# Optimization experiments

Hardware: AMD Instinct MI355X
Metric: run time of the kernel (lower is better)

Reference implementation:

```python
import jax, jax.numpy as jnp
import numpy as np

# Channel layout assumed by the model's CH dict
CH_ELEV, CH_WS, CH_WD, CH_HUM, CH_NDVI, CH_FIRE = 0, 1, 2, 3, 4, 5
P_BURN, W_WIND, W_SLOPE = 0.58, 0.045, 0.078
OFFSETS = [(-1, 0), (-1, 1), (0, 1), (1, 1), (1, 0), (1, -1), (0, -1), (-1, -1)]
DIR_ANGLES = [90.0, 45.0, 0.0, 315.0, 270.0, 225.0, 180.0, 135.0]
SOBEL_X = np.array([[-1, 0, 1], [-2, 0, 2], [-1, 0, 1]], np.float32) / 8.0
SOBEL_Y = np.array([[-1, -2, -1], [0, 0, 0], [1, 2, 1]], np.float32) / 8.0


def setup_inputs() -> dict:
    key = jax.random.key(0)
    x = jax.random.uniform(key, (16, 6, 1024, 1024), dtype=jnp.float32)
    return {"x": x}


def _conv2d_same(img, k):
    # img: (B,1,H,W), k: (3,3)
    kern = jnp.asarray(k).reshape(1, 1, 3, 3)
    return jax.lax.conv_general_dilated(img, kern, (1, 1), ((1, 1), (1, 1)))


def _shift(mask, dr, dc):
    # mask: (B,H,W) float; zero-padded shift matching torch slicing
    B, H, W = mask.shape
    p = jnp.pad(mask, ((0, 0), (1, 1), (1, 1)))
    return p[:, 1 + dr:1 + dr + H, 1 + dc:1 + dc + W]


def reference(x):
    B, C, H, W = x.shape
    elev = x[:, CH_ELEV:CH_ELEV + 1]          # (B,1,H,W)
    ws = x[:, CH_WS]                           # (B,H,W)
    wd = x[:, CH_WD]
    hum = x[:, CH_HUM]
    ndvi = x[:, CH_NDVI]
    fs = x[:, CH_FIRE]

    dx = _conv2d_same(elev, SOBEL_X)
    dy = _conv2d_same(elev, SOBEL_Y)
    grad_mag = jnp.sqrt(dx * dx + dy * dy + 1e-8)
    slope = (jnp.arctan(grad_mag) * (180.0 / np.pi))[:, 0]  # (B,H,W) degrees

    burning = (fs > 0.5).astype(x.dtype)
    wind_math = jnp.mod(270.0 - wd, 360.0)
    slope_effect = 1.0 + W_SLOPE * jnp.tan(slope * (np.pi / 180.0))
    moisture_damp = jnp.clip(1.0 - 2.0 * hum * 200.0, 0.3, 1.0)
    veg_factor = 0.5 + 0.5 * jnp.clip(ndvi, 0.0, 1.0)
    base = P_BURN * slope_effect * moisture_damp * veg_factor  # wind-independent part

    prob = jnp.zeros((B, H, W), dtype=x.dtype)
    for (dr, dc), d_angle in zip(OFFSETS, DIR_ANGLES):
        shifted = _shift(burning, dr, dc)
        angle_diff = (d_angle - wind_math) * (np.pi / 180.0)
        wind_factor = 1.0 + W_WIND * jnp.cos(angle_diff) * ws
        p_spread = jnp.clip(base * wind_factor, 0.0, 1.0)
        prob = jnp.maximum(prob, shifted * p_spread)

    unburned = (fs < 0.5).astype(x.dtype)
    out = jnp.maximum(fs, prob * unburned)
    return out[:, None]  # (B,1,H,W)
```

## Files before the change

### kernel.cpp

```cpp
#include <hip/hip_runtime.h>

namespace {
constexpr int CH = 6;
constexpr int H  = 1024;
constexpr int W  = 1024;
constexpr float P_BURN  = 0.58f;
constexpr float W_WIND  = 0.045f;
constexpr float W_SLOPE = 0.078f;
constexpr float C45     = 0.70710678118654752f;
constexpr float DEG2RAD = 0.017453292519943295f;

__device__ __forceinline__ void load6(const float* __restrict__ plane, int row,
                                      int j0, float v[6]) {
    if ((unsigned)row >= (unsigned)H) {
        v[0] = v[1] = v[2] = v[3] = v[4] = v[5] = 0.f;
        return;
    }
    const float* r = plane + (size_t)row * W;
    const float4 m = *reinterpret_cast<const float4*>(r + j0);
    v[0] = (j0 > 0)     ? r[j0 - 1] : 0.f;
    v[1] = m.x; v[2] = m.y; v[3] = m.z; v[4] = m.w;
    v[5] = (j0 + 4 < W) ? r[j0 + 4] : 0.f;
}
}

__global__ __launch_bounds__(256)
void fire_step(const float* __restrict__ x, float* __restrict__ out, int B) {
    const int W4  = W / 4;
    const int gid = blockIdx.x * 256 + threadIdx.x;
    const int j0  = (gid % W4) * 4;
    const int rest = gid / W4;
    const int i = rest % H;
    const int b = rest / H;
    if (b >= B) return;

    const size_t plane = (size_t)H * W;
    const float* base_b = x + (size_t)b * CH * plane;
    const float* elev  = base_b + 0 * plane;
    const float* wsp   = base_b + 1 * plane;
    const float* wdp   = base_b + 2 * plane;
    const float* hump  = base_b + 3 * plane;
    const float* ndvip = base_b + 4 * plane;
    const float* fsp   = base_b + 5 * plane;

    float em[6], ec[6], ep[6];
    load6(elev, i - 1, j0, em);
    load6(elev, i,     j0, ec);
    load6(elev, i + 1, j0, ep);
    float fm[6], fc[6], fq[6];
    load6(fsp, i - 1, j0, fm);
    load6(fsp, i,     j0, fc);
    load6(fsp, i + 1, j0, fq);

    const size_t roff = (size_t)i * W + j0;
    const float4 ws4 = *reinterpret_cast<const float4*>(wsp   + roff);
    const float4 wd4 = *reinterpret_cast<const float4*>(wdp   + roff);
    const float4 hu4 = *reinterpret_cast<const float4*>(hump  + roff);
    const float4 nd4 = *reinterpret_cast<const float4*>(ndvip + roff);
    const float* wsa = reinterpret_cast<const float*>(&ws4);
    const float* wda = reinterpret_cast<const float*>(&wd4);
    const float* hua = reinterpret_cast<const float*>(&hu4);
    const float* nda = reinterpret_cast<const float*>(&nd4);

    float o[4];
#pragma unroll
    for (int k = 0; k < 4; ++k) {
        const float dx = ((em[k+2] - em[k]) + 2.f * (ec[k+2] - ec[k]) +
                          (ep[k+2] - ep[k])) * 0.125f;
        const float dy = ((ep[k]   - em[k]) + 2.f * (ep[k+1] - em[k+1]) +
                          (ep[k+2] - em[k+2])) * 0.125f;
        const float g = sqrtf(dx * dx + dy * dy + 1e-8f);
        const float slope_eff = 1.f + W_SLOPE * g;
        const float moist = fminf(fmaxf(1.f - 400.f * hua[k], 0.3f), 1.f);
        const float veg   = 0.5f + 0.5f * fminf(fmaxf(nda[k], 0.f), 1.f);
        const float basep = P_BURN * slope_eff * moist * veg;

        const float wrad = fmodf(270.f - wda[k], 360.f) * DEG2RAD;
        float sw, cw;
        __sincosf(wrad, &sw, &cw);

        float best = -2.f;
        if (fm[k+1] > 0.5f) best = fmaxf(best,  sw);
        if (fm[k+2] > 0.5f) best = fmaxf(best,  C45 * (cw + sw));
        if (fc[k+2] > 0.5f) best = fmaxf(best,  cw);
        if (fq[k+2] > 0.5f) best = fmaxf(best,  C45 * (cw - sw));
        if (fq[k+1] > 0.5f) best = fmaxf(best, -sw);
        if (fq[k]   > 0.5f) best = fmaxf(best, -C45 * (cw + sw));
        if (fc[k]   > 0.5f) best = fmaxf(best, -cw);
        if (fm[k]   > 0.5f) best = fmaxf(best,  C45 * (sw - cw));

        float prob = 0.f;
        if (best > -1.5f) {
            const float wf = 1.f + W_WIND * best * wsa[k];
            prob = fminf(fmaxf(basep * wf, 0.f), 1.f);
        }
        const float fsc = fc[k + 1];
        o[k] = fmaxf(fsc, (fsc < 0.5f) ? prob : 0.f);
    }

    float4 ov;
    ov.x = o[0]; ov.y = o[1]; ov.z = o[2]; ov.w = o[3];
    *reinterpret_cast<float4*>(out + (size_t)b * plane + roff) = ov;
}

extern "C" void kernel_launch(void* const* d_in, const int* in_sizes, int n_in,
                              void* d_out, int out_size, void* d_ws, size_t ws_size,
                              hipStream_t stream) {
    const float* x = (const float*)d_in[0];
    float* out = (float*)d_out;
    const int B = in_sizes[0] / (CH * H * W);
    const int total_threads = B * H * (W / 4);
    const int blocks = (total_threads + 255) / 256;
    fire_step<<<blocks, 256, 0, stream>>>(x, out, B);
}
```

Before: 527.0 us.

## Process four rows per thread with rolling row registers and shuffle halos

Each thread now computes four consecutive output rows and keeps the previous and current elevation and fire rows in registers as a rolling window, so each row of the stencil channels is loaded about once per thread instead of three times. Horizontal halo values now come from neighbouring lanes via shuffles, with scalar loads only at wavefront edges. The fmod on wind direction is dropped because sin and cos are periodic. The cost is a quarter as many threads and more registers per thread, which may lower occupancy and latency hiding on this memory-bound kernel.

```diff
diff --git a/kernel.cpp b/kernel.cpp
--- a/kernel.cpp
+++ b/kernel.cpp
@@ -4,34 +4,44 @@
 constexpr int CH = 6;
 constexpr int H  = 1024;
 constexpr int W  = 1024;
+constexpr int ROWS = 4;
 constexpr float P_BURN  = 0.58f;
 constexpr float W_WIND  = 0.045f;
 constexpr float W_SLOPE = 0.078f;
 constexpr float C45     = 0.70710678118654752f;
 constexpr float DEG2RAD = 0.017453292519943295f;
 
-__device__ __forceinline__ void load6(const float* __restrict__ plane, int row,
-                                      int j0, float v[6]) {
+struct Row6 { float v[6]; };
+
+__device__ __forceinline__ Row6 load_row(const float* __restrict__ plane,
+                                         int row, int j0, int lane) {
+    Row6 r;
     if ((unsigned)row >= (unsigned)H) {
-        v[0] = v[1] = v[2] = v[3] = v[4] = v[5] = 0.f;
-        return;
+#pragma unroll
+        for (int t = 0; t < 6; ++t) r.v[t] = 0.f;
+        return r;
     }
-    const float* r = plane + (size_t)row * W;
-    const float4 m = *reinterpret_cast<const float4*>(r + j0);
-    v[0] = (j0 > 0)     ? r[j0 - 1] : 0.f;
-    v[1] = m.x; v[2] = m.y; v[3] = m.z; v[4] = m.w;
-    v[5] = (j0 + 4 < W) ? r[j0 + 4] : 0.f;
+    const float* p = plane + (size_t)row * W;
+    const float4 m = *reinterpret_cast<const float4*>(p + j0);
+    float left  = __shfl_up(m.w, 1);
+    float right = __shfl_down(m.x, 1);
+    if (lane == 0)  left  = (j0 > 0)     ? p[j0 - 1] : 0.f;
+    if (lane == 63) right = (j0 + 4 < W) ? p[j0 + 4] : 0.f;
+    r.v[0] = left; r.v[1] = m.x; r.v[2] = m.y; r.v[3] = m.z; r.v[4] = m.w;
+    r.v[5] = right;
+    return r;
 }
 }
 
 __global__ __launch_bounds__(256)
 void fire_step(const float* __restrict__ x, float* __restrict__ out, int B) {
-    const int W4  = W / 4;
-    const int gid = blockIdx.x * 256 + threadIdx.x;
-    const int j0  = (gid % W4) * 4;
+    const int W4 = W / 4;
+    const int lane = threadIdx.x & 63;
+    const int gid  = blockIdx.x * 256 + threadIdx.x;
+    const int j0   = (gid % W4) * 4;
     const int rest = gid / W4;
-    const int i = rest % H;
-    const int b = rest / H;
+    const int i0   = (rest % (H / ROWS)) * ROWS;
+    const int b    = rest / (H / ROWS);
     if (b >= B) return;
 
     const size_t plane = (size_t)H * W;
@@ -42,65 +52,71 @@
     const float* hump  = base_b + 3 * plane;
     const float* ndvip = base_b + 4 * plane;
     const float* fsp   = base_b + 5 * plane;
+    float* outp = out + (size_t)b * plane;
 
-    float em[6], ec[6], ep[6];
-    load6(elev, i - 1, j0, em);
-    load6(elev, i,     j0, ec);
-    load6(elev, i + 1, j0, ep);
-    float fm[6], fc[6], fq[6];
-    load6(fsp, i - 1, j0, fm);
-    load6(fsp, i,     j0, fc);
-    load6(fsp, i + 1, j0, fq);
+    Row6 em = load_row(elev, i0 - 1, j0, lane);
+    Row6 ec = load_row(elev, i0,     j0, lane);
+    Row6 fm = load_row(fsp,  i0 - 1, j0, lane);
+    Row6 fc = load_row(fsp,  i0,     j0, lane);
 
-    const size_t roff = (size_t)i * W + j0;
-    const float4 ws4 = *reinterpret_cast<const float4*>(wsp   + roff);
-    const float4 wd4 = *reinterpret_cast<const float4*>(wdp   + roff);
-    const float4 hu4 = *reinterpret_cast<const float4*>(hump  + roff);
-    const float4 nd4 = *reinterpret_cast<const float4*>(ndvip + roff);
-    const float* wsa = reinterpret_cast<const float*>(&ws4);
-    const float* wda = reinterpret_cast<const float*>(&wd4);
-    const float* hua = reinterpret_cast<const float*>(&hu4);
-    const float* nda = reinterpret_cast<const float*>(&nd4);
+#pragma unroll
+    for (int r = 0; r < ROWS; ++r) {
+        const int i = i0 + r;
+        const Row6 ep = load_row(elev, i + 1, j0, lane);
+        const Row6 fq = load_row(fsp,  i + 1, j0, lane);
 
-    float o[4];
+        const size_t roff = (size_t)i * W + j0;
+        const float4 ws4 = *reinterpret_cast<const float4*>(wsp   + roff);
+        const float4 wd4 = *reinterpret_cast<const float4*>(wdp   + roff);
+        const float4 hu4 = *reinterpret_cast<const float4*>(hump  + roff);
+        const float4 nd4 = *reinterpret_cast<const float4*>(ndvip + roff);
+        const float* wsa = reinterpret_cast<const float*>(&ws4);
+        const float* wda = reinterpret_cast<const float*>(&wd4);
+        const float* hua = reinterpret_cast<const float*>(&hu4);
+        const float* nda = reinterpret_cast<const float*>(&nd4);
+
+        float o[4];
 #pragma unroll
-    for (int k = 0; k < 4; ++k) {
-        const float dx = ((em[k+2] - em[k]) + 2.f * (ec[k+2] - ec[k]) +
-                          (ep[k+2] - ep[k])) * 0.125f;
-        const float dy = ((ep[k]   - em[k]) + 2.f * (ep[k+1] - em[k+1]) +
-                          (ep[k+2] - em[k+2])) * 0.125f;
-        const float g = sqrtf(dx * dx + dy * dy + 1e-8f);
-        const float slope_eff = 1.f + W_SLOPE * g;
-        const float moist = fminf(fmaxf(1.f - 400.f * hua[k], 0.3f), 1.f);
-        const float veg   = 0.5f + 0.5f * fminf(fmaxf(nda[k], 0.f), 1.f);
-        const float basep = P_BURN * slope_eff * moist * veg;
+        for (int k = 0; k < 4; ++k) {
+            const float dx = ((em.v[k+2] - em.v[k]) + 2.f * (ec.v[k+2] - ec.v[k]) +
+                              (ep.v[k+2] - ep.v[k])) * 0.125f;
+            const float dy = ((ep.v[k]   - em.v[k]) + 2.f * (ep.v[k+1] - em.v[k+1]) +
+                              (ep.v[k+2] - em.v[k+2])) * 0.125f;
+            const float g = sqrtf(dx * dx + dy * dy + 1e-8f);
+            const float slope_eff = 1.f + W_SLOPE * g;
+            const float moist = fminf(fmaxf(1.f - 400.f * hua[k], 0.3f), 1.f);
+            const float veg   = 0.5f + 0.5f * fminf(fmaxf(nda[k], 0.f), 1.f);
+            const float basep = P_BURN * slope_eff * moist * veg;
 
-        const float wrad = fmodf(270.f - wda[k], 360.f) * DEG2RAD;
-        float sw, cw;
-        __sincosf(wrad, &sw, &cw);
+            const float wrad = (270.f - wda[k]) * DEG2RAD;
+            float sw, cw;
+            __sincosf(wrad, &sw, &cw);
 
-        float best = -2.f;
-        if (fm[k+1] > 0.5f) best = fmaxf(best,  sw);
-        if (fm[k+2] > 0.5f) best = fmaxf(best,  C45 * (cw + sw));
-        if (fc[k+2] > 0.5f) best = fmaxf(best,  cw);
-        if (fq[k+2] > 0.5f) best = fmaxf(best,  C45 * (cw - sw));
-        if (fq[k+1] > 0.5f) best = fmaxf(best, -sw);
-        if (fq[k]   > 0.5f) best = fmaxf(best, -C45 * (cw + sw));
-        if (fc[k]   > 0.5f) best = fmaxf(best, -cw);
-        if (fm[k]   > 0.5f) best = fmaxf(best,  C45 * (sw - cw));
+            float best = -2.f;
+            if (fm.v[k+1] > 0.5f) best = fmaxf(best,  sw);
+            if (fm.v[k+2] > 0.5f) best = fmaxf(best,  C45 * (cw + sw));
+            if (fc.v[k+2] > 0.5f) best = fmaxf(best,  cw);
+            if (fq.v[k+2] > 0.5f) best = fmaxf(best,  C45 * (cw - sw));
+            if (fq.v[k+1] > 0.5f) best = fmaxf(best, -sw);
+            if (fq.v[k]   > 0.5f) best = fmaxf(best, -C45 * (cw + sw));
+            if (fc.v[k]   > 0.5f) best = fmaxf(best, -cw);
+            if (fm.v[k]   > 0.5f) best = fmaxf(best,  C45 * (sw - cw));
 
-        float prob = 0.f;
-        if (best > -1.5f) {
-            const float wf = 1.f + W_WIND * best * wsa[k];
-            prob = fminf(fmaxf(basep * wf, 0.f), 1.f);
+            float prob = 0.f;
+            if (best > -1.5f) {
+                const float wf = 1.f + W_WIND * best * wsa[k];
+                prob = fminf(fmaxf(basep * wf, 0.f), 1.f);
+            }
+            const float fsc = fc.v[k + 1];
+            o[k] = fmaxf(fsc, (fsc < 0.5f) ? prob : 0.f);
         }
-        const float fsc = fc[k + 1];
-        o[k] = fmaxf(fsc, (fsc < 0.5f) ? prob : 0.f);
+
+        float4 ov;
+        ov.x = o[0]; ov.y = o[1]; ov.z = o[2]; ov.w = o[3];
+        *reinterpret_cast<float4*>(outp + roff) = ov;
+
+        em = ec; ec = ep; fm = fc; fc = fq;
     }
-
-    float4 ov;
-    ov.x = o[0]; ov.y = o[1]; ov.z = o[2]; ov.w = o[3];
-    *reinterpret_cast<float4*>(out + (size_t)b * plane + roff) = ov;
 }
 
 extern "C" void kernel_launch(void* const* d_in, const int* in_sizes, int n_in,
@@ -109,7 +125,7 @@
     const float* x = (const float*)d_in[0];
     float* out = (float*)d_out;
     const int B = in_sizes[0] / (CH * H * W);
-    const int total_threads = B * H * (W / 4);
+    const int total_threads = B * (H / ROWS) * (W / 4);
     const int blocks = (total_threads + 255) / 256;
     fire_step<<<blocks, 256, 0, stream>>>(x, out, B);
 }
```

Result: no change. 534.9 us (+1.5%).
